# Performance work log

Measured on AMD Instinct MI355X. Metric: run time of the kernel, lower is better.

## Reference

```python
import jax, jax.numpy as jnp
import numpy as np

B, SY, SX, D = 16, 2048, 2048, 128

def setup_inputs() -> dict:
    key = jax.random.key(0)
    kx, ky = jax.random.split(key)
    input_x = jax.random.normal(kx, (B, SX, D), dtype=jnp.float32)
    input_y = jax.random.normal(ky, (B, SY, D), dtype=jnp.float32)
    return {"input_x": input_x, "input_y": input_y}

def reference(input_x, input_y):
    # attention_matrix: [B, SY, SX] = y @ x^T
    attention_matrix = jnp.einsum('byd,bxd->byx', input_y, input_x)
    # softmax over x-sequence (dim=2)
    attention_weight = jax.nn.softmax(attention_matrix, axis=2)
    # visual: mean of raw scores over y-sequence (dim=1) -> [B, SX]
    attention_visual = jnp.mean(attention_matrix, axis=1)
    # out: weighted sum of x then mean over y-sequence -> [B, D]
    attention_out = jnp.einsum('byx,bxd->byd', attention_weight, input_x)
    attention_out = jnp.mean(attention_out, axis=1)
    return (attention_visual, attention_out)
```

## Files before the change

kernel.cpp:

```cpp
#include <hip/hip_runtime.h>
#include <math.h>

constexpr int Bn = 16, SY = 2048, SX = 2048, Dd = 128;
constexpr int XT = 64;
constexpr int NXT = SX / XT;
constexpr int PIT = 72;
constexpr float INV_N = 1.0f / 2048.0f;
constexpr size_t NE = (size_t)Bn * SY * Dd;

using half8  = __attribute__((ext_vector_type(8))) _Float16;
using half4  = __attribute__((ext_vector_type(4))) _Float16;
using floatx4 = __attribute__((ext_vector_type(4))) float;

#define DPP_ROR(v, ctrl) __int_as_float(__builtin_amdgcn_update_dpp( \
    __float_as_int(v), __float_as_int(v), (ctrl), 0xf, 0xf, false))

__device__ __forceinline__ float rowmax16(float v) {
  v = fmaxf(v, DPP_ROR(v, 0x121));
  v = fmaxf(v, DPP_ROR(v, 0x122));
  v = fmaxf(v, DPP_ROR(v, 0x124));
  v = fmaxf(v, DPP_ROR(v, 0x128));
  return v;
}
__device__ __forceinline__ float rowsum16(float v) {
  v += DPP_ROR(v, 0x121);
  v += DPP_ROR(v, 0x122);
  v += DPP_ROR(v, 0x124);
  v += DPP_ROR(v, 0x128);
  return v;
}

__device__ __forceinline__ float sel4(const float* a, int q) {
  float r = a[0];
  r = (q == 1) ? a[1] : r;
  r = (q == 2) ? a[2] : r;
  r = (q == 3) ? a[3] : r;
  return r;
}

__device__ __forceinline__ void gld_lds16(const _Float16* g, _Float16* l) {
  __builtin_amdgcn_global_load_lds(
      (const __attribute__((address_space(1))) void*)g,
      (__attribute__((address_space(3))) void*)l, 16, 0, 0);
}

__global__ void xprep_kernel(const float* __restrict__ x,
                             _Float16* __restrict__ x16, _Float16* __restrict__ xT16) {
  __shared__ _Float16 lt[128 * PIT];
  const int t = threadIdx.x;
  const int b = blockIdx.x >> 5, rb = blockIdx.x & 31;
  const float* xp = x + ((size_t)b * SX + rb * 64) * Dd;
  _Float16* x16p = x16 + ((size_t)b * SX + rb * 64) * Dd;
  #pragma unroll
  for (int it = 0; it < 8; ++it) {
    int tau = it * 256 + t;
    int row = tau >> 5, c4 = tau & 31;
    floatx4 f = *(const floatx4*)(xp + row * Dd + 4 * c4);
    half4 h;
    h[0]=(_Float16)f[0]; h[1]=(_Float16)f[1]; h[2]=(_Float16)f[2]; h[3]=(_Float16)f[3];
    *(half4*)(x16p + row * Dd + 4 * c4) = h;
    #pragma unroll
    for (int j = 0; j < 4; ++j) lt[(4 * c4 + j) * PIT + row] = h[j];
  }
  __syncthreads();
  #pragma unroll
  for (int it = 0; it < 4; ++it) {
    int tau = it * 256 + t;
    int d = tau >> 3, g = tau & 7;
    half8 h = *(const half8*)&lt[d * PIT + g * 8];
    *(half8*)(xT16 + (size_t)(b * Dd + d) * SX + rb * 64 + g * 8) = h;
  }
}

__launch_bounds__(256, 2)
__global__ void attn_kernel(const _Float16* __restrict__ x16, const _Float16* __restrict__ xT16,
                            const float* __restrict__ y,
                            float* __restrict__ out_ws, float* __restrict__ ysump) {
  __shared__ _Float16 xrm[2][64 * 128];
  __shared__ _Float16 xtp[2][128 * 64];
  __shared__ _Float16 Pw[4][16 * PIT];
  __shared__ float ysw[4][128];
  __shared__ float cbuf[4][128];

  const int t = threadIdx.x;
  const int w = t >> 6, lane = t & 63;
  const int n = lane & 15, q = lane >> 4;
  const int xcd = blockIdx.x & 7, kk = blockIdx.x >> 3;
  const int b = (xcd << 1) | (kk & 1);
  const int yblk = kk >> 1;
  const int y0 = yblk * 64;

  const float* yrow = y + (size_t)(b * SY + y0 + w * 16 + n) * Dd;
  half8 afrag[4];
  {
    float yv[4][8];
    #pragma unroll
    for (int k = 0; k < 4; ++k) {
      floatx4 f0 = *(const floatx4*)(yrow + k * 32 + q * 8);
      floatx4 f1 = *(const floatx4*)(yrow + k * 32 + q * 8 + 4);
      half8 h;
      h[0]=(_Float16)f0[0]; h[1]=(_Float16)f0[1]; h[2]=(_Float16)f0[2]; h[3]=(_Float16)f0[3];
      h[4]=(_Float16)f1[0]; h[5]=(_Float16)f1[1]; h[6]=(_Float16)f1[2]; h[7]=(_Float16)f1[3];
      afrag[k] = h;
      #pragma unroll
      for (int j = 0; j < 4; ++j) { yv[k][j] = f0[j]; yv[k][4 + j] = f1[j]; }
    }
    #pragma unroll
    for (int k = 0; k < 4; ++k)
      #pragma unroll
      for (int j = 0; j < 8; ++j) {
        float s = rowsum16(yv[k][j]);
        if (n == 0) ysw[w][k * 32 + q * 8 + j] = s;
      }
  }

  half8 ones;
  #pragma unroll
  for (int j = 0; j < 8; ++j) ones[j] = (_Float16)1.0f;

  float m_r[4];
  floatx4 acc_o[8], lacc;
  #pragma unroll
  for (int r = 0; r < 4; ++r) m_r[r] = -INFINITY;
  #pragma unroll
  for (int d = 0; d < 8; ++d) acc_o[d] = (floatx4){0, 0, 0, 0};
  lacc = (floatx4){0, 0, 0, 0};

  const _Float16* xb  = x16  + (size_t)b * SX * Dd;
  const _Float16* xTb = xT16 + (size_t)b * Dd * SX;
  _Float16* P = Pw[w];

  int l_off[4], off_rm[4], off_xt[4];
  #pragma unroll
  for (int ii = 0; ii < 4; ++ii) {
    int G = (w * 4 + ii) * 64 + lane;
    l_off[ii] = G * 8;
    { int row = G >> 4, gs = G & 15, g = (gs - row) & 15;
      off_rm[ii] = row * 128 + g * 8; }
    { int row = G >> 3, gs = G & 7, g = (gs - row) & 7;
      off_xt[ii] = row * SX + g * 8; }
  }

  #pragma unroll
  for (int ii = 0; ii < 4; ++ii) {
    gld_lds16(xb + off_rm[ii], &xrm[0][l_off[ii]]);
    gld_lds16(xTb + off_xt[ii], &xtp[0][l_off[ii]]);
  }
  __syncthreads();

  for (int it = 0; it < NXT; ++it) {
    const int cur = it & 1;

    if (it + 1 < NXT) {
      const _Float16* xsrc  = xb + (size_t)(it + 1) * XT * Dd;
      const _Float16* xTsrc = xTb + (it + 1) * XT;
      #pragma unroll
      for (int ii = 0; ii < 4; ++ii) {
        gld_lds16(xsrc + off_rm[ii], &xrm[cur ^ 1][l_off[ii]]);
        gld_lds16(xTsrc + off_xt[ii], &xtp[cur ^ 1][l_off[ii]]);
      }
    }

    floatx4 s[4];
    #pragma unroll
    for (int c = 0; c < 4; ++c) s[c] = (floatx4){0, 0, 0, 0};
    #pragma unroll
    for (int k = 0; k < 4; ++k) {
      half8 bf[4];
      #pragma unroll
      for (int c = 0; c < 4; ++c) {
        int row = 16 * c + n;
        int sw = (k * 4 + q + row) & 15;
        bf[c] = *(const half8*)&xrm[cur][row * 128 + sw * 8];
      }
      #pragma unroll
      for (int c = 0; c < 4; ++c)
        s[c] = __builtin_amdgcn_mfma_f32_16x16x32_f16(afrag[k], bf[c], s[c], 0, 0, 0);
    }

    float mt[4], al[4];
    #pragma unroll
    for (int r = 0; r < 4; ++r) {
      float mv = fmaxf(fmaxf(s[0][r], s[1][r]), fmaxf(s[2][r], s[3][r]));
      mv = rowmax16(mv);
      mt[r] = fmaxf(m_r[r], mv);
      al[r] = __expf(m_r[r] - mt[r]);
      m_r[r] = mt[r];
    }
    #pragma unroll
    for (int r = 0; r < 4; ++r) {
      #pragma unroll
      for (int c = 0; c < 4; ++c)
        P[(4 * q + r) * PIT + 16 * c + n] = (_Float16)__expf(s[c][r] - mt[r]);
      lacc[r] *= al[r];
      #pragma unroll
      for (int d = 0; d < 8; ++d) acc_o[d][r] *= al[r];
    }

    #pragma unroll
    for (int k2 = 0; k2 < 2; ++k2) {
      half8 pf = *(const half8*)&P[n * PIT + k2 * 32 + q * 8];
      lacc = __builtin_amdgcn_mfma_f32_16x16x32_f16(pf, ones, lacc, 0, 0, 0);
      #pragma unroll
      for (int d = 0; d < 8; ++d) {
        int row = 16 * d + n;
        int sw = (k2 * 4 + q + row) & 7;
        half8 xf = *(const half8*)&xtp[cur][row * 64 + sw * 8];
        acc_o[d] = __builtin_amdgcn_mfma_f32_16x16x32_f16(pf, xf, acc_o[d], 0, 0, 0);
      }
    }

    __syncthreads();
  }

  float inv_l[4];
  #pragma unroll
  for (int r = 0; r < 4; ++r) inv_l[r] = 1.f / lacc[r];
  float ps[8];
  #pragma unroll
  for (int d = 0; d < 8; ++d) {
    float s = acc_o[d][0] * inv_l[0] + acc_o[d][1] * inv_l[1] +
              acc_o[d][2] * inv_l[2] + acc_o[d][3] * inv_l[3];
    s += __shfl_xor(s, 16);
    s += __shfl_xor(s, 32);
    ps[d] = s;
  }
  cbuf[w][16 * q + n]      = sel4(ps, q);
  cbuf[w][64 + 16 * q + n] = sel4(ps + 4, q);
  __syncthreads();
  if (t < 128) {
    float s = 0.f, yp = 0.f;
    #pragma unroll
    for (int i = 0; i < 4; ++i) { s += cbuf[i][t]; yp += ysw[i][t]; }
    out_ws[(size_t)(b * 32 + yblk) * 128 + t] = s;
    ysump[(size_t)(b * 32 + yblk) * 128 + t] = yp;
  }
}

__global__ void finale_kernel(const _Float16* __restrict__ x16, const float* __restrict__ ysump,
                              const float* __restrict__ out_ws,
                              float* __restrict__ visual, float* __restrict__ out) {
  const int t = threadIdx.x, blk = blockIdx.x;
  if (blk < 128) {
    __shared__ float ysum[128];
    const int b = blk >> 3, x0 = (blk & 7) * 256;
    if (t < 128) {
      float s = 0.f;
      #pragma unroll
      for (int j = 0; j < 32; ++j) s += ysump[(size_t)(b * 32 + j) * 128 + t];
      ysum[t] = s;
    }
    __syncthreads();
    const int x = x0 + t;
    const _Float16* xr = x16 + ((size_t)b * SX + x) * Dd;
    float dot = 0.f;
    #pragma unroll
    for (int g = 0; g < 16; ++g) {
      half8 h = *(const half8*)(xr + g * 8);
      #pragma unroll
      for (int j = 0; j < 8; ++j) dot += ysum[g * 8 + j] * (float)h[j];
    }
    visual[(size_t)b * SX + x] = dot * INV_N;
  } else {
    #pragma unroll
    for (int i = 0; i < 8; ++i) {
      int e = i * 256 + t;
      int bb = e >> 7, d = e & 127;
      float s = 0.f;
      for (int j = 0; j < 32; ++j) s += out_ws[(size_t)(bb * 32 + j) * 128 + d];
      out[bb * 128 + d] = s * INV_N;
    }
  }
}

extern "C" void kernel_launch(void* const* d_in, const int* in_sizes, int n_in,
                              void* d_out, int out_size, void* d_ws, size_t ws_size,
                              hipStream_t stream) {
  const float* x = (const float*)d_in[0];
  const float* y = (const float*)d_in[1];
  float* visual = (float*)d_out;
  float* out    = (float*)d_out + (size_t)Bn * SX;

  _Float16* x16  = (_Float16*)d_ws;
  _Float16* xT16 = x16 + NE;
  float* wsf    = (float*)(xT16 + NE);
  float* out_ws = wsf;
  float* ysump  = wsf + (size_t)512 * 128;

  xprep_kernel<<<512, 256, 0, stream>>>(x, x16, xT16);
  attn_kernel<<<512, 256, 0, stream>>>(x16, xT16, y, out_ws, ysump);
  finale_kernel<<<129, 256, 0, stream>>>(x16, ysump, out_ws, visual, out);
}
```

Baseline: 150.9 us.

## Split x sequence across warp pairs with 32-row y tiles and merged softmax stats

Each warp now handles 32 y rows instead of 16. Warp pairs split the x sequence into two halves, each pair running its own online softmax. At the end the partial max and sum values are merged through shared memory. Each warp loads 8 async copies of one matrix type per iteration, with x tiles of 32 and a new swizzle. This raises register reuse of the B fragments (each x fragment feeds two MFMAs), at the cost of more accumulator registers and a cross-warp merge step.

```diff
diff --git a/kernel.cpp b/kernel.cpp
--- a/kernel.cpp
+++ b/kernel.cpp
@@ -2,9 +2,9 @@
 #include <math.h>
 
 constexpr int Bn = 16, SY = 2048, SX = 2048, Dd = 128;
-constexpr int XT = 64;
-constexpr int NXT = SX / XT;
+constexpr int XT = 32;
 constexpr int PIT = 72;
+constexpr int PP = 40;
 constexpr float INV_N = 1.0f / 2048.0f;
 constexpr size_t NE = (size_t)Bn * SY * Dd;
 
@@ -76,41 +76,50 @@
 __global__ void attn_kernel(const _Float16* __restrict__ x16, const _Float16* __restrict__ xT16,
                             const float* __restrict__ y,
                             float* __restrict__ out_ws, float* __restrict__ ysump) {
-  __shared__ _Float16 xrm[2][64 * 128];
-  __shared__ _Float16 xtp[2][128 * 64];
-  __shared__ _Float16 Pw[4][16 * PIT];
-  __shared__ float ysw[4][128];
+  __shared__ _Float16 xrm[2][2][32 * 128];
+  __shared__ _Float16 xtp[2][2][128 * 32];
+  __shared__ _Float16 Pw[4][32 * PP];
+  __shared__ float ml_m[4][32], ml_l[4][32];
+  __shared__ float ysw[2][128];
   __shared__ float cbuf[4][128];
 
   const int t = threadIdx.x;
   const int w = t >> 6, lane = t & 63;
   const int n = lane & 15, q = lane >> 4;
+  const int ygrp = w >> 1, chunk = w & 1;
   const int xcd = blockIdx.x & 7, kk = blockIdx.x >> 3;
   const int b = (xcd << 1) | (kk & 1);
   const int yblk = kk >> 1;
   const int y0 = yblk * 64;
 
-  const float* yrow = y + (size_t)(b * SY + y0 + w * 16 + n) * Dd;
-  half8 afrag[4];
+  half8 afrag[2][4];
   {
-    float yv[4][8];
-    #pragma unroll
-    for (int k = 0; k < 4; ++k) {
-      floatx4 f0 = *(const floatx4*)(yrow + k * 32 + q * 8);
-      floatx4 f1 = *(const floatx4*)(yrow + k * 32 + q * 8 + 4);
-      half8 h;
-      h[0]=(_Float16)f0[0]; h[1]=(_Float16)f0[1]; h[2]=(_Float16)f0[2]; h[3]=(_Float16)f0[3];
-      h[4]=(_Float16)f1[0]; h[5]=(_Float16)f1[1]; h[6]=(_Float16)f1[2]; h[7]=(_Float16)f1[3];
-      afrag[k] = h;
-      #pragma unroll
-      for (int j = 0; j < 4; ++j) { yv[k][j] = f0[j]; yv[k][4 + j] = f1[j]; }
-    }
+    float yss[4][8];
     #pragma unroll
     for (int k = 0; k < 4; ++k)
       #pragma unroll
+      for (int j = 0; j < 8; ++j) yss[k][j] = 0.f;
+    #pragma unroll
+    for (int s = 0; s < 2; ++s) {
+      const float* yrow = y + (size_t)(b * SY + y0 + ygrp * 32 + s * 16 + n) * Dd;
+      #pragma unroll
+      for (int k = 0; k < 4; ++k) {
+        floatx4 f0 = *(const floatx4*)(yrow + k * 32 + q * 8);
+        floatx4 f1 = *(const floatx4*)(yrow + k * 32 + q * 8 + 4);
+        half8 h;
+        h[0]=(_Float16)f0[0]; h[1]=(_Float16)f0[1]; h[2]=(_Float16)f0[2]; h[3]=(_Float16)f0[3];
+        h[4]=(_Float16)f1[0]; h[5]=(_Float16)f1[1]; h[6]=(_Float16)f1[2]; h[7]=(_Float16)f1[3];
+        afrag[s][k] = h;
+        #pragma unroll
+        for (int j = 0; j < 4; ++j) { yss[k][j] += f0[j]; yss[k][4 + j] += f1[j]; }
+      }
+    }
+    #pragma unroll
+    for (int k = 0; k < 4; ++k)
+      #pragma unroll
       for (int j = 0; j < 8; ++j) {
-        float s = rowsum16(yv[k][j]);
-        if (n == 0) ysw[w][k * 32 + q * 8 + j] = s;
+        float v = rowsum16(yss[k][j]);
+        if (chunk == 0 && n == 0) ysw[ygrp][k * 32 + q * 8 + j] = v;
       }
   }
 
@@ -118,122 +127,157 @@
   #pragma unroll
   for (int j = 0; j < 8; ++j) ones[j] = (_Float16)1.0f;
 
-  float m_r[4];
-  floatx4 acc_o[8], lacc;
-  #pragma unroll
-  for (int r = 0; r < 4; ++r) m_r[r] = -INFINITY;
-  #pragma unroll
-  for (int d = 0; d < 8; ++d) acc_o[d] = (floatx4){0, 0, 0, 0};
-  lacc = (floatx4){0, 0, 0, 0};
+  float m_r[2][4];
+  floatx4 acc_o[2][8], lacc[2];
+  #pragma unroll
+  for (int s = 0; s < 2; ++s) {
+    #pragma unroll
+    for (int r = 0; r < 4; ++r) m_r[s][r] = -INFINITY;
+    #pragma unroll
+    for (int d = 0; d < 8; ++d) acc_o[s][d] = (floatx4){0, 0, 0, 0};
+    lacc[s] = (floatx4){0, 0, 0, 0};
+  }
 
   const _Float16* xb  = x16  + (size_t)b * SX * Dd;
   const _Float16* xTb = xT16 + (size_t)b * Dd * SX;
   _Float16* P = Pw[w];
 
-  int l_off[4], off_rm[4], off_xt[4];
-  #pragma unroll
-  for (int ii = 0; ii < 4; ++ii) {
-    int G = (w * 4 + ii) * 64 + lane;
+  const int RL = w >> 1, RC = w & 1;
+  int l_off[8];
+  size_t boff[8];
+  #pragma unroll
+  for (int ii = 0; ii < 8; ++ii) {
+    int G = ii * 64 + lane;
     l_off[ii] = G * 8;
-    { int row = G >> 4, gs = G & 15, g = (gs - row) & 15;
-      off_rm[ii] = row * 128 + g * 8; }
-    { int row = G >> 3, gs = G & 7, g = (gs - row) & 7;
-      off_xt[ii] = row * SX + g * 8; }
-  }
-
-  #pragma unroll
-  for (int ii = 0; ii < 4; ++ii) {
-    gld_lds16(xb + off_rm[ii], &xrm[0][l_off[ii]]);
-    gld_lds16(xTb + off_xt[ii], &xtp[0][l_off[ii]]);
-  }
+    if (RL == 0) { int row = G >> 4, g = ((G & 15) - row) & 15;
+                   boff[ii] = (size_t)row * 128 + g * 8; }
+    else         { int row = G >> 2, g = ((G & 3) - (row >> 2)) & 3;
+                   boff[ii] = (size_t)row * SX + g * 8; }
+  }
+  const _Float16* gbase = RL ? (xTb + (size_t)RC * 1024)
+                             : (xb + (size_t)RC * 1024 * 128);
+  const size_t gstep = RL ? (size_t)XT : (size_t)XT * 128;
+  _Float16* lbase = RL ? &xtp[RC][0][0] : &xrm[RC][0][0];
+
+  #pragma unroll
+  for (int ii = 0; ii < 8; ++ii)
+    gld_lds16(gbase + boff[ii], lbase + l_off[ii]);
   __syncthreads();
 
-  for (int it = 0; it < NXT; ++it) {
+  for (int it = 0; it < 32; ++it) {
     const int cur = it & 1;
 
-    if (it + 1 < NXT) {
-      const _Float16* xsrc  = xb + (size_t)(it + 1) * XT * Dd;
-      const _Float16* xTsrc = xTb + (it + 1) * XT;
-      #pragma unroll
-      for (int ii = 0; ii < 4; ++ii) {
-        gld_lds16(xsrc + off_rm[ii], &xrm[cur ^ 1][l_off[ii]]);
-        gld_lds16(xTsrc + off_xt[ii], &xtp[cur ^ 1][l_off[ii]]);
-      }
-    }
-
-    floatx4 s[4];
-    #pragma unroll
-    for (int c = 0; c < 4; ++c) s[c] = (floatx4){0, 0, 0, 0};
+    if (it + 1 < 32) {
+      const _Float16* gp = gbase + (size_t)(it + 1) * gstep;
+      _Float16* lp = lbase + (cur ^ 1) * 4096;
+      #pragma unroll
+      for (int ii = 0; ii < 8; ++ii)
+        gld_lds16(gp + boff[ii], lp + l_off[ii]);
+    }
+
+    floatx4 sA[2][2];
+    #pragma unroll
+    for (int s = 0; s < 2; ++s) { sA[s][0] = (floatx4){0,0,0,0}; sA[s][1] = (floatx4){0,0,0,0}; }
     #pragma unroll
     for (int k = 0; k < 4; ++k) {
-      half8 bf[4];
-      #pragma unroll
-      for (int c = 0; c < 4; ++c) {
+      half8 bf[2];
+      #pragma unroll
+      for (int c = 0; c < 2; ++c) {
         int row = 16 * c + n;
         int sw = (k * 4 + q + row) & 15;
-        bf[c] = *(const half8*)&xrm[cur][row * 128 + sw * 8];
-      }
-      #pragma unroll
-      for (int c = 0; c < 4; ++c)
-        s[c] = __builtin_amdgcn_mfma_f32_16x16x32_f16(afrag[k], bf[c], s[c], 0, 0, 0);
-    }
-
-    float mt[4], al[4];
+        bf[c] = *(const half8*)&xrm[chunk][cur][row * 128 + sw * 8];
+      }
+      #pragma unroll
+      for (int s = 0; s < 2; ++s)
+        #pragma unroll
+        for (int c = 0; c < 2; ++c)
+          sA[s][c] = __builtin_amdgcn_mfma_f32_16x16x32_f16(afrag[s][k], bf[c], sA[s][c], 0, 0, 0);
+    }
+
+    #pragma unroll
+    for (int s = 0; s < 2; ++s) {
+      float mt[4], al[4];
+      #pragma unroll
+      for (int r = 0; r < 4; ++r) {
+        float mv = fmaxf(sA[s][0][r], sA[s][1][r]);
+        mv = rowmax16(mv);
+        mt[r] = fmaxf(m_r[s][r], mv);
+        al[r] = __expf(m_r[s][r] - mt[r]);
+        m_r[s][r] = mt[r];
+      }
+      #pragma unroll
+      for (int r = 0; r < 4; ++r) {
+        #pragma unroll
+        for (int c = 0; c < 2; ++c)
+          P[(s * 16 + 4 * q + r) * PP + 16 * c + n] = (_Float16)__expf(sA[s][c][r] - mt[r]);
+        lacc[s][r] *= al[r];
+        #pragma unroll
+        for (int d = 0; d < 8; ++d) acc_o[s][d][r] *= al[r];
+      }
+    }
+
+    half8 pf[2];
+    #pragma unroll
+    for (int s = 0; s < 2; ++s)
+      pf[s] = *(const half8*)&P[(s * 16 + n) * PP + q * 8];
+    #pragma unroll
+    for (int s = 0; s < 2; ++s)
+      lacc[s] = __builtin_amdgcn_mfma_f32_16x16x32_f16(pf[s], ones, lacc[s], 0, 0, 0);
+    #pragma unroll
+    for (int d = 0; d < 8; ++d) {
+      int row = 16 * d + n;
+      int sw = (q + (row >> 2)) & 3;
+      half8 xf = *(const half8*)&xtp[chunk][cur][row * 32 + sw * 8];
+      #pragma unroll
+      for (int s = 0; s < 2; ++s)
+        acc_o[s][d] = __builtin_amdgcn_mfma_f32_16x16x32_f16(pf[s], xf, acc_o[s][d], 0, 0, 0);
+    }
+
+    __syncthreads();
+  }
+
+  if (n == 0) {
+    #pragma unroll
+    for (int s = 0; s < 2; ++s)
+      #pragma unroll
+      for (int r = 0; r < 4; ++r) {
+        ml_m[w][s * 16 + 4 * q + r] = m_r[s][r];
+        ml_l[w][s * 16 + 4 * q + r] = lacc[s][r];
+      }
+  }
+  __syncthreads();
+  const int p = w ^ 1;
+  float scale[2][4];
+  #pragma unroll
+  for (int s = 0; s < 2; ++s)
     #pragma unroll
     for (int r = 0; r < 4; ++r) {
-      float mv = fmaxf(fmaxf(s[0][r], s[1][r]), fmaxf(s[2][r], s[3][r]));
-      mv = rowmax16(mv);
-      mt[r] = fmaxf(m_r[r], mv);
-      al[r] = __expf(m_r[r] - mt[r]);
-      m_r[r] = mt[r];
-    }
-    #pragma unroll
-    for (int r = 0; r < 4; ++r) {
-      #pragma unroll
-      for (int c = 0; c < 4; ++c)
-        P[(4 * q + r) * PIT + 16 * c + n] = (_Float16)__expf(s[c][r] - mt[r]);
-      lacc[r] *= al[r];
-      #pragma unroll
-      for (int d = 0; d < 8; ++d) acc_o[d][r] *= al[r];
-    }
-
-    #pragma unroll
-    for (int k2 = 0; k2 < 2; ++k2) {
-      half8 pf = *(const half8*)&P[n * PIT + k2 * 32 + q * 8];
-      lacc = __builtin_amdgcn_mfma_f32_16x16x32_f16(pf, ones, lacc, 0, 0, 0);
-      #pragma unroll
-      for (int d = 0; d < 8; ++d) {
-        int row = 16 * d + n;
-        int sw = (k2 * 4 + q + row) & 7;
-        half8 xf = *(const half8*)&xtp[cur][row * 64 + sw * 8];
-        acc_o[d] = __builtin_amdgcn_mfma_f32_16x16x32_f16(pf, xf, acc_o[d], 0, 0, 0);
-      }
-    }
-
-    __syncthreads();
-  }
-
-  float inv_l[4];
-  #pragma unroll
-  for (int r = 0; r < 4; ++r) inv_l[r] = 1.f / lacc[r];
+      int rr = s * 16 + 4 * q + r;
+      float mp = ml_m[p][rr], lp = ml_l[p][rr];
+      float M = fmaxf(m_r[s][r], mp);
+      float f = __expf(m_r[s][r] - M), fp = __expf(mp - M);
+      scale[s][r] = f / (f * lacc[s][r] + fp * lp);
+    }
+
   float ps[8];
   #pragma unroll
   for (int d = 0; d < 8; ++d) {
-    float s = acc_o[d][0] * inv_l[0] + acc_o[d][1] * inv_l[1] +
-              acc_o[d][2] * inv_l[2] + acc_o[d][3] * inv_l[3];
-    s += __shfl_xor(s, 16);
-    s += __shfl_xor(s, 32);
-    ps[d] = s;
+    float v = 0.f;
+    #pragma unroll
+    for (int s = 0; s < 2; ++s)
+      #pragma unroll
+      for (int r = 0; r < 4; ++r) v += scale[s][r] * acc_o[s][d][r];
+    v += __shfl_xor(v, 16);
+    v += __shfl_xor(v, 32);
+    ps[d] = v;
   }
   cbuf[w][16 * q + n]      = sel4(ps, q);
   cbuf[w][64 + 16 * q + n] = sel4(ps + 4, q);
   __syncthreads();
   if (t < 128) {
-    float s = 0.f, yp = 0.f;
-    #pragma unroll
-    for (int i = 0; i < 4; ++i) { s += cbuf[i][t]; yp += ysw[i][t]; }
+    float s = cbuf[0][t] + cbuf[1][t] + cbuf[2][t] + cbuf[3][t];
     out_ws[(size_t)(b * 32 + yblk) * 128 + t] = s;
-    ysump[(size_t)(b * 32 + yblk) * 128 + t] = yp;
+    ysump[(size_t)(b * 32 + yblk) * 128 + t] = ysw[0][t] + ysw[1][t];
   }
 }
 
```

Measured after the change: 159.1 us. +5.4%, slower.
